# Performance work log

Measured on AMD Instinct MI355X. Metric: run time of the kernel, lower is better.

## Reference

```python
import jax, jax.numpy as jnp
import numpy as np

N = 8192
IN_F = 256
OUT_F = 128


def setup_inputs() -> dict:
    key = jax.random.key(0)
    k1, k2, k3, k4, k5, k6 = jax.random.split(key, 6)
    input = jax.random.normal(k1, (N, IN_F), dtype=jnp.float32)
    adj = jax.random.randint(k2, (N, N), 0, 2, dtype=jnp.int32)
    # xavier-uniform-like init scaled by gain=0.5
    def xavier(k, shape, gain=0.5):
        fan_in, fan_out = shape[0], shape[1]
        lim = gain * np.sqrt(6.0 / (fan_in + fan_out))
        return jax.random.uniform(k, shape, dtype=jnp.float32, minval=-lim, maxval=lim)
    W_s = xavier(k3, (IN_F, OUT_F))
    a_s = xavier(k4, (OUT_F, 1))
    W_n = xavier(k5, (IN_F, OUT_F))
    a_n = xavier(k6, (OUT_F, 1))
    return {"input": input, "adj": adj, "W_s": W_s, "a_s": a_s, "W_n": W_n, "a_n": a_n}


def reference(input, adj, W_s, a_s, W_n, a_n):
    # Projections: [N, out_features]
    h_s = input @ W_s
    h_n = input @ W_n
    # Additive attention logits: e[i, j] = relu((h_s @ a_s)[i] + (h_n @ a_n)[j])
    e = jax.nn.relu((h_s @ a_s) + (h_n @ a_n).T)  # [N, N]
    # Masked softmax over neighbors (dim=1)
    attention = jnp.where(adj > 0, e, jnp.float32(-9e15))
    attention = jax.nn.softmax(attention, axis=1)
    # Self-scaling term (sum of softmax rows, kept for faithfulness)
    attention_sum = jnp.sum(attention, axis=-1, keepdims=True)
    attention_s = 1.0 / (1.0 + attention_sum)
    # Dropout is identity in eval mode (p=0 / training=False)
    h_prime = attention_s * h_s + attention @ h_n
    # concat=True -> elu activation
    return jax.nn.elu(h_prime)
```

## Files before the change

kernel.cpp:

```cpp
#include <hip/hip_runtime.h>
#include <math.h>

#define NN 8192

typedef short short8 __attribute__((ext_vector_type(8)));
typedef float f32x4 __attribute__((ext_vector_type(4)));

__device__ __forceinline__ float eluf(float x) {
  return x > 0.f ? x : (__expf(x) - 1.f);
}
__device__ __forceinline__ unsigned short f2bf(float f) {
  union { float f; unsigned u; } v; v.f = f;
  unsigned r = v.u + 0x7fffu + ((v.u >> 16) & 1u);
  return (unsigned short)(r >> 16);
}
__device__ __forceinline__ unsigned pack4(int4 v, int sh) {
  return ((unsigned)(v.x & 1) << sh) | ((unsigned)(v.y & 1) << (sh + 1)) |
         ((unsigned)(v.z & 1) << (sh + 2)) | ((unsigned)(v.w & 1) << (sh + 3));
}

__global__ __launch_bounds__(256) void k_pre(const float* __restrict__ X,
                                             const int* __restrict__ A,
                                             const float* __restrict__ Ws,
                                             const float* __restrict__ Wn,
                                             const float* __restrict__ as_,
                                             const float* __restrict__ an_,
                                             float* __restrict__ Hs,
                                             unsigned short* __restrict__ HnT,
                                             float* __restrict__ es_out,
                                             float* __restrict__ en_out,
                                             unsigned* __restrict__ P) {
  __shared__ float4 lin4[8 * 64];
  const int bid = blockIdx.x;
  const int q5 = bid / 5, r5 = bid - q5 * 5;
  const int t = threadIdx.x;

  if (r5 == 4) {
    const int row0 = q5 * 32;
#pragma unroll 1
    for (int k = 0; k < 32; ++k) {
      int g = t + k * 256;
      int rr = g >> 8;
      int c8 = g & 255;
      const int4* src = (const int4*)(A + (size_t)(row0 + rr) * NN + c8 * 32);
      int4 v0 = src[0], v1 = src[1], v2 = src[2], v3 = src[3];
      int4 v4 = src[4], v5 = src[5], v6 = src[6], v7 = src[7];
      unsigned w = pack4(v0, 0)  | pack4(v1, 4)  | pack4(v2, 8)  | pack4(v3, 12) |
                   pack4(v4, 16) | pack4(v5, 20) | pack4(v6, 24) | pack4(v7, 28);
      P[(size_t)(row0 + rr) * 256 + c8] = w;
    }
    return;
  }

  const int i0 = (q5 * 4 + r5) * 8;
  const float4* Xg = (const float4*)X + (size_t)i0 * 64;
  lin4[t] = Xg[t];
  lin4[t + 256] = Xg[t + 256];
  __syncthreads();
  const int c = t & 127;
  const int rh = t >> 7;
  float accs[4], accn[4];
#pragma unroll
  for (int r = 0; r < 4; ++r) { accs[r] = 0.f; accn[r] = 0.f; }
  for (int k = 0; k < 256; k += 4) {
    float ws0 = Ws[(k + 0) * 128 + c], ws1 = Ws[(k + 1) * 128 + c];
    float ws2 = Ws[(k + 2) * 128 + c], ws3 = Ws[(k + 3) * 128 + c];
    float wn0 = Wn[(k + 0) * 128 + c], wn1 = Wn[(k + 1) * 128 + c];
    float wn2 = Wn[(k + 2) * 128 + c], wn3 = Wn[(k + 3) * 128 + c];
#pragma unroll
    for (int r = 0; r < 4; ++r) {
      float4 iv = lin4[(rh * 4 + r) * 64 + (k >> 2)];
      accs[r] = fmaf(iv.x, ws0, accs[r]); accs[r] = fmaf(iv.y, ws1, accs[r]);
      accs[r] = fmaf(iv.z, ws2, accs[r]); accs[r] = fmaf(iv.w, ws3, accs[r]);
      accn[r] = fmaf(iv.x, wn0, accn[r]); accn[r] = fmaf(iv.y, wn1, accn[r]);
      accn[r] = fmaf(iv.z, wn2, accn[r]); accn[r] = fmaf(iv.w, wn3, accn[r]);
    }
  }
#pragma unroll
  for (int r = 0; r < 4; ++r)
    Hs[(size_t)(i0 + rh * 4 + r) * 128 + c] = accs[r];
  {
    union { unsigned short us[4]; ushort4 u4; } pk;
#pragma unroll
    for (int r = 0; r < 4; ++r) pk.us[r] = f2bf(accn[r]);
    *(ushort4*)(HnT + (size_t)(i0 >> 3) * 1024 + c * 8 + rh * 4) = pk.u4;
  }
  float* red = (float*)lin4;
  const int wv = t >> 6, ln = t & 63;
  __syncthreads();
  {
    float av = as_[c];
#pragma unroll
    for (int r = 0; r < 4; ++r) red[(rh * 4 + r) * 128 + c] = accs[r] * av;
  }
  __syncthreads();
#pragma unroll
  for (int h = 0; h < 2; ++h) {
    int row = wv * 2 + h;
    float p = red[row * 128 + ln] + red[row * 128 + 64 + ln];
#pragma unroll
    for (int off = 32; off >= 1; off >>= 1) p += __shfl_down(p, off);
    if (ln == 0) es_out[i0 + row] = __expf(p);
  }
  __syncthreads();
  {
    float av = an_[c];
#pragma unroll
    for (int r = 0; r < 4; ++r) red[(rh * 4 + r) * 128 + c] = accn[r] * av;
  }
  __syncthreads();
#pragma unroll
  for (int h = 0; h < 2; ++h) {
    int row = wv * 2 + h;
    float p = red[row * 128 + ln] + red[row * 128 + 64 + ln];
#pragma unroll
    for (int off = 32; off >= 1; off >>= 1) p += __shfl_down(p, off);
    if (ln == 0) en_out[i0 + row] = __expf(p);
  }
}

__global__ __launch_bounds__(512, 4) void k_main(const unsigned* __restrict__ Pk,
                                                 const unsigned short* __restrict__ HnT,
                                                 const float* __restrict__ es_g,
                                                 const float* __restrict__ en_g,
                                                 float* __restrict__ HsOut) {
  __shared__ __align__(16) char smem[49152];
  float* en_lds = (float*)smem;
  unsigned* bits_lds = (unsigned*)(smem + 32768);
  float* cmb = (float*)smem;
  __shared__ float zsh[8][16];
  __shared__ float zf[16];

  const int t = threadIdx.x;
  const int wv = t >> 6;
  const int ln = t & 63;
  const int q = ln >> 4;
  const int m = ln & 15;
  const int row0 = blockIdx.x * 16;

  {
    float4* dst = (float4*)en_lds;
    const float4* s4 = (const float4*)en_g;
#pragma unroll
    for (int k = 0; k < 4; ++k) dst[t + k * 512] = s4[t + k * 512];
#pragma unroll
    for (int k = 0; k < 8; ++k) {
      int g = t + k * 512;
      int rr = g >> 8;
      int c8 = g & 255;
      unsigned w = Pk[(size_t)(row0 + rr) * 256 + c8];
      bits_lds[(c8 >> 5) * 512 + (c8 & 31) * 16 + rr] = w;
    }
  }

  const float sme = es_g[row0 + m];
  const unsigned short* bptr = HnT + ((size_t)(wv * 128 + q) * 128 + m) * 8;
  const float* nvl = en_lds + wv * 1024 + q * 8;
  const unsigned* bts = bits_lds + wv * 512 + m;

  f32x4 acc[8];
#pragma unroll
  for (int ft = 0; ft < 8; ++ft) acc[ft] = (f32x4){0.f, 0.f, 0.f, 0.f};
  float zp = 0.f;

  union Breg { uint4 u; short8 s; };
  Breg breg[8];

  __syncthreads();

  breg[0].u = *(const uint4*)(bptr);       breg[1].u = *(const uint4*)(bptr + 128);
  breg[2].u = *(const uint4*)(bptr + 256); breg[3].u = *(const uint4*)(bptr + 384);
  breg[4].u = *(const uint4*)(bptr + 512); breg[5].u = *(const uint4*)(bptr + 640);
  breg[6].u = *(const uint4*)(bptr + 768); breg[7].u = *(const uint4*)(bptr + 896);

#pragma unroll 2
  for (int tt = 0; tt < 32; ++tt) {
    short8 fr;
    {
      float4 nv0 = *(const float4*)(nvl + tt * 32);
      float4 nv1 = *(const float4*)(nvl + tt * 32 + 4);
      const unsigned bw = bts[tt * 16];
      const unsigned byte = (bw >> (q * 8)) & 0xffu;
      float ev[8] = {nv0.x, nv0.y, nv0.z, nv0.w, nv1.x, nv1.y, nv1.z, nv1.w};
#pragma unroll
      for (int k = 0; k < 8; ++k) {
        float w = ((byte >> k) & 1u) ? fmaxf(sme * ev[k], 1.f) : 0.f;
        zp += w;
        fr[k] = (short)f2bf(w);
      }
    }
    __builtin_amdgcn_s_setprio(1);
    acc[0] = __builtin_amdgcn_mfma_f32_16x16x32_bf16(fr, breg[0].s, acc[0], 0, 0, 0);
    acc[1] = __builtin_amdgcn_mfma_f32_16x16x32_bf16(fr, breg[1].s, acc[1], 0, 0, 0);
    acc[2] = __builtin_amdgcn_mfma_f32_16x16x32_bf16(fr, breg[2].s, acc[2], 0, 0, 0);
    acc[3] = __builtin_amdgcn_mfma_f32_16x16x32_bf16(fr, breg[3].s, acc[3], 0, 0, 0);
    acc[4] = __builtin_amdgcn_mfma_f32_16x16x32_bf16(fr, breg[4].s, acc[4], 0, 0, 0);
    acc[5] = __builtin_amdgcn_mfma_f32_16x16x32_bf16(fr, breg[5].s, acc[5], 0, 0, 0);
    acc[6] = __builtin_amdgcn_mfma_f32_16x16x32_bf16(fr, breg[6].s, acc[6], 0, 0, 0);
    acc[7] = __builtin_amdgcn_mfma_f32_16x16x32_bf16(fr, breg[7].s, acc[7], 0, 0, 0);
    __builtin_amdgcn_s_setprio(0);
    {
      const unsigned short* p = bptr + (size_t)(tt + 1) * 4096;
      breg[0].u = *(const uint4*)(p);       breg[1].u = *(const uint4*)(p + 128);
      breg[2].u = *(const uint4*)(p + 256); breg[3].u = *(const uint4*)(p + 384);
      breg[4].u = *(const uint4*)(p + 512); breg[5].u = *(const uint4*)(p + 640);
      breg[6].u = *(const uint4*)(p + 768); breg[7].u = *(const uint4*)(p + 896);
    }
  }

  {
    float zz = zp;
    zz += __shfl_down(zz, 32);
    zz += __shfl_down(zz, 16);
    if (ln < 16) zsh[wv][ln] = zz;
  }
  __syncthreads();
  if (wv >= 4) {
#pragma unroll
    for (int ft = 0; ft < 8; ++ft)
#pragma unroll
      for (int reg = 0; reg < 4; ++reg)
        cmb[(wv - 4) * 2048 + (q * 4 + reg) * 128 + ft * 16 + m] = acc[ft][reg];
  }
  __syncthreads();
  if (wv < 4) {
#pragma unroll
    for (int ft = 0; ft < 8; ++ft)
#pragma unroll
      for (int reg = 0; reg < 4; ++reg)
        acc[ft][reg] += cmb[wv * 2048 + (q * 4 + reg) * 128 + ft * 16 + m];
  }
  __syncthreads();
  if (wv < 4) {
#pragma unroll
    for (int ft = 0; ft < 8; ++ft)
#pragma unroll
      for (int reg = 0; reg < 4; ++reg)
        cmb[wv * 2048 + (q * 4 + reg) * 128 + ft * 16 + m] = acc[ft][reg];
  }
  if (t < 16) {
    float z = zsh[0][t] + zsh[1][t] + zsh[2][t] + zsh[3][t] +
              zsh[4][t] + zsh[5][t] + zsh[6][t] + zsh[7][t];
    zf[t] = 1.f / z;
  }
  __syncthreads();
  {
    const int row = t >> 5;
    const int f0 = (t & 31) * 4;
    f32x4 ssum = *(const f32x4*)&cmb[row * 128 + f0];
#pragma unroll
    for (int w = 1; w < 4; ++w) ssum += *(const f32x4*)&cmb[w * 2048 + row * 128 + f0];
    const float invz = zf[row];
    const size_t off = (size_t)(row0 + row) * 128 + f0;
    float4 h = *(const float4*)(HsOut + off);
    float4 o;
    o.x = eluf(fmaf(ssum[0], invz, 0.5f * h.x));
    o.y = eluf(fmaf(ssum[1], invz, 0.5f * h.y));
    o.z = eluf(fmaf(ssum[2], invz, 0.5f * h.z));
    o.w = eluf(fmaf(ssum[3], invz, 0.5f * h.w));
    *(float4*)(HsOut + off) = o;
  }
}

extern "C" void kernel_launch(void* const* d_in, const int* in_sizes, int n_in,
                              void* d_out, int out_size, void* d_ws, size_t ws_size,
                              hipStream_t stream) {
  const float* X   = (const float*)d_in[0];
  const int*   A   = (const int*)d_in[1];
  const float* Ws  = (const float*)d_in[2];
  const float* as_ = (const float*)d_in[3];
  const float* Wn  = (const float*)d_in[4];
  const float* an_ = (const float*)d_in[5];
  float* out = (float*)d_out;

  unsigned short* HnT = (unsigned short*)d_ws;
  float* es = (float*)(HnT + (size_t)128 * NN);
  float* en = es + NN;
  unsigned* P = (unsigned*)(en + NN);

  k_pre<<<1280, 256, 0, stream>>>(X, A, Ws, Wn, as_, an_, out, HnT, es, en, P);
  k_main<<<512, 512, 0, stream>>>(P, HnT, es, en, out);
}
```

Baseline: 418.3 us.

## Process 32 rows per block with 1024 threads, reusing B fragments across two row tiles

Each block of k_main now handles 32 output rows with 16 waves arranged as 2 feature halves by 8 column chunks. Each wave reuses its loaded HnT fragments for two 16-row A tiles, which halves global reads of the HnT matrix per output row. The cross-wave reduction becomes a multi-stage tree through LDS with more barriers. The grid shrinks to 256 blocks, which may leave compute units underfilled on a 256-CU part, and the 64KB LDS plus doubled register state may limit occupancy.

Result: no change. 421.5 us (+0.8%).

```diff
diff --git a/kernel.cpp b/kernel.cpp
--- a/kernel.cpp
+++ b/kernel.cpp
@@ -119,137 +119,156 @@
   }
 }
 
-__global__ __launch_bounds__(512, 4) void k_main(const unsigned* __restrict__ Pk,
-                                                 const unsigned short* __restrict__ HnT,
-                                                 const float* __restrict__ es_g,
-                                                 const float* __restrict__ en_g,
-                                                 float* __restrict__ HsOut) {
-  __shared__ __align__(16) char smem[49152];
+__global__ __launch_bounds__(1024, 4) void k_main(const unsigned* __restrict__ Pk,
+                                                  const unsigned short* __restrict__ HnT,
+                                                  const float* __restrict__ es_g,
+                                                  const float* __restrict__ en_g,
+                                                  float* __restrict__ HsOut) {
+  __shared__ __align__(16) char smem[65536];
   float* en_lds = (float*)smem;
   unsigned* bits_lds = (unsigned*)(smem + 32768);
   float* cmb = (float*)smem;
-  __shared__ float zsh[8][16];
-  __shared__ float zf[16];
+  __shared__ float zsh[8][32];
+  __shared__ float zf[32];
 
   const int t = threadIdx.x;
   const int wv = t >> 6;
+  const int fp = wv >> 3;
+  const int jp = wv & 7;
   const int ln = t & 63;
   const int q = ln >> 4;
   const int m = ln & 15;
-  const int row0 = blockIdx.x * 16;
+  const int row0 = blockIdx.x * 32;
 
   {
     float4* dst = (float4*)en_lds;
     const float4* s4 = (const float4*)en_g;
-#pragma unroll
-    for (int k = 0; k < 4; ++k) dst[t + k * 512] = s4[t + k * 512];
+    dst[t] = s4[t];
+    dst[t + 1024] = s4[t + 1024];
 #pragma unroll
     for (int k = 0; k < 8; ++k) {
-      int g = t + k * 512;
+      int g = t + k * 1024;
       int rr = g >> 8;
       int c8 = g & 255;
       unsigned w = Pk[(size_t)(row0 + rr) * 256 + c8];
-      bits_lds[(c8 >> 5) * 512 + (c8 & 31) * 16 + rr] = w;
-    }
-  }
-
-  const float sme = es_g[row0 + m];
-  const unsigned short* bptr = HnT + ((size_t)(wv * 128 + q) * 128 + m) * 8;
-  const float* nvl = en_lds + wv * 1024 + q * 8;
-  const unsigned* bts = bits_lds + wv * 512 + m;
-
-  f32x4 acc[8];
-#pragma unroll
-  for (int ft = 0; ft < 8; ++ft) acc[ft] = (f32x4){0.f, 0.f, 0.f, 0.f};
-  float zp = 0.f;
+      bits_lds[(c8 >> 5) * 1024 + (c8 & 31) * 32 + rr] = w;
+    }
+  }
+
+  const float sme0 = es_g[row0 + m];
+  const float sme1 = es_g[row0 + 16 + m];
+  const unsigned short* bptr = HnT + ((size_t)(jp * 128 + q) * 128 + fp * 64 + m) * 8;
+  const float* nvl = en_lds + jp * 1024 + q * 8;
+  const unsigned* bts = bits_lds + jp * 1024 + m;
+
+  f32x4 acc0[4], acc1[4];
+#pragma unroll
+  for (int ftl = 0; ftl < 4; ++ftl) {
+    acc0[ftl] = (f32x4){0.f, 0.f, 0.f, 0.f};
+    acc1[ftl] = (f32x4){0.f, 0.f, 0.f, 0.f};
+  }
+  float zp0 = 0.f, zp1 = 0.f;
 
   union Breg { uint4 u; short8 s; };
-  Breg breg[8];
-
-  __syncthreads();
-
-  breg[0].u = *(const uint4*)(bptr);       breg[1].u = *(const uint4*)(bptr + 128);
-  breg[2].u = *(const uint4*)(bptr + 256); breg[3].u = *(const uint4*)(bptr + 384);
-  breg[4].u = *(const uint4*)(bptr + 512); breg[5].u = *(const uint4*)(bptr + 640);
-  breg[6].u = *(const uint4*)(bptr + 768); breg[7].u = *(const uint4*)(bptr + 896);
+  Breg breg[4];
+
+  __syncthreads();
+
+  breg[0].u = *(const uint4*)(bptr);
+  breg[1].u = *(const uint4*)(bptr + 128);
+  breg[2].u = *(const uint4*)(bptr + 256);
+  breg[3].u = *(const uint4*)(bptr + 384);
 
 #pragma unroll 2
   for (int tt = 0; tt < 32; ++tt) {
-    short8 fr;
+    short8 fr0, fr1;
     {
       float4 nv0 = *(const float4*)(nvl + tt * 32);
       float4 nv1 = *(const float4*)(nvl + tt * 32 + 4);
-      const unsigned bw = bts[tt * 16];
-      const unsigned byte = (bw >> (q * 8)) & 0xffu;
+      const unsigned bw0 = bts[tt * 32];
+      const unsigned bw1 = bts[tt * 32 + 16];
+      const unsigned byte0 = (bw0 >> (q * 8)) & 0xffu;
+      const unsigned byte1 = (bw1 >> (q * 8)) & 0xffu;
       float ev[8] = {nv0.x, nv0.y, nv0.z, nv0.w, nv1.x, nv1.y, nv1.z, nv1.w};
 #pragma unroll
       for (int k = 0; k < 8; ++k) {
-        float w = ((byte >> k) & 1u) ? fmaxf(sme * ev[k], 1.f) : 0.f;
-        zp += w;
-        fr[k] = (short)f2bf(w);
+        float w0 = ((byte0 >> k) & 1u) ? fmaxf(sme0 * ev[k], 1.f) : 0.f;
+        float w1 = ((byte1 >> k) & 1u) ? fmaxf(sme1 * ev[k], 1.f) : 0.f;
+        zp0 += w0; zp1 += w1;
+        fr0[k] = (short)f2bf(w0);
+        fr1[k] = (short)f2bf(w1);
       }
     }
     __builtin_amdgcn_s_setprio(1);
-    acc[0] = __builtin_amdgcn_mfma_f32_16x16x32_bf16(fr, breg[0].s, acc[0], 0, 0, 0);
-    acc[1] = __builtin_amdgcn_mfma_f32_16x16x32_bf16(fr, breg[1].s, acc[1], 0, 0, 0);
-    acc[2] = __builtin_amdgcn_mfma_f32_16x16x32_bf16(fr, breg[2].s, acc[2], 0, 0, 0);
-    acc[3] = __builtin_amdgcn_mfma_f32_16x16x32_bf16(fr, breg[3].s, acc[3], 0, 0, 0);
-    acc[4] = __builtin_amdgcn_mfma_f32_16x16x32_bf16(fr, breg[4].s, acc[4], 0, 0, 0);
-    acc[5] = __builtin_amdgcn_mfma_f32_16x16x32_bf16(fr, breg[5].s, acc[5], 0, 0, 0);
-    acc[6] = __builtin_amdgcn_mfma_f32_16x16x32_bf16(fr, breg[6].s, acc[6], 0, 0, 0);
-    acc[7] = __builtin_amdgcn_mfma_f32_16x16x32_bf16(fr, breg[7].s, acc[7], 0, 0, 0);
+    acc0[0] = __builtin_amdgcn_mfma_f32_16x16x32_bf16(fr0, breg[0].s, acc0[0], 0, 0, 0);
+    acc1[0] = __builtin_amdgcn_mfma_f32_16x16x32_bf16(fr1, breg[0].s, acc1[0], 0, 0, 0);
+    acc0[1] = __builtin_amdgcn_mfma_f32_16x16x32_bf16(fr0, breg[1].s, acc0[1], 0, 0, 0);
+    acc1[1] = __builtin_amdgcn_mfma_f32_16x16x32_bf16(fr1, breg[1].s, acc1[1], 0, 0, 0);
+    acc0[2] = __builtin_amdgcn_mfma_f32_16x16x32_bf16(fr0, breg[2].s, acc0[2], 0, 0, 0);
+    acc1[2] = __builtin_amdgcn_mfma_f32_16x16x32_bf16(fr1, breg[2].s, acc1[2], 0, 0, 0);
+    acc0[3] = __builtin_amdgcn_mfma_f32_16x16x32_bf16(fr0, breg[3].s, acc0[3], 0, 0, 0);
+    acc1[3] = __builtin_amdgcn_mfma_f32_16x16x32_bf16(fr1, breg[3].s, acc1[3], 0, 0, 0);
     __builtin_amdgcn_s_setprio(0);
     {
       const unsigned short* p = bptr + (size_t)(tt + 1) * 4096;
-      breg[0].u = *(const uint4*)(p);       breg[1].u = *(const uint4*)(p + 128);
-      breg[2].u = *(const uint4*)(p + 256); breg[3].u = *(const uint4*)(p + 384);
-      breg[4].u = *(const uint4*)(p + 512); breg[5].u = *(const uint4*)(p + 640);
-      breg[6].u = *(const uint4*)(p + 768); breg[7].u = *(const uint4*)(p + 896);
-    }
-  }
-
-  {
-    float zz = zp;
-    zz += __shfl_down(zz, 32);
-    zz += __shfl_down(zz, 16);
-    if (ln < 16) zsh[wv][ln] = zz;
-  }
-  __syncthreads();
-  if (wv >= 4) {
-#pragma unroll
-    for (int ft = 0; ft < 8; ++ft)
-#pragma unroll
-      for (int reg = 0; reg < 4; ++reg)
-        cmb[(wv - 4) * 2048 + (q * 4 + reg) * 128 + ft * 16 + m] = acc[ft][reg];
-  }
-  __syncthreads();
-  if (wv < 4) {
-#pragma unroll
-    for (int ft = 0; ft < 8; ++ft)
-#pragma unroll
-      for (int reg = 0; reg < 4; ++reg)
-        acc[ft][reg] += cmb[wv * 2048 + (q * 4 + reg) * 128 + ft * 16 + m];
-  }
-  __syncthreads();
-  if (wv < 4) {
-#pragma unroll
-    for (int ft = 0; ft < 8; ++ft)
-#pragma unroll
-      for (int reg = 0; reg < 4; ++reg)
-        cmb[wv * 2048 + (q * 4 + reg) * 128 + ft * 16 + m] = acc[ft][reg];
-  }
-  if (t < 16) {
+      breg[0].u = *(const uint4*)(p);
+      breg[1].u = *(const uint4*)(p + 128);
+      breg[2].u = *(const uint4*)(p + 256);
+      breg[3].u = *(const uint4*)(p + 384);
+    }
+  }
+
+  {
+    float zz0 = zp0, zz1 = zp1;
+    zz0 += __shfl_down(zz0, 32); zz0 += __shfl_down(zz0, 16);
+    zz1 += __shfl_down(zz1, 32); zz1 += __shfl_down(zz1, 16);
+    if (fp == 0 && ln < 16) { zsh[jp][m] = zz0; zsh[jp][16 + m] = zz1; }
+  }
+  __syncthreads();
+
+#define DUMP_SLOT(S)                                                        \
+  {                                                                         \
+    float* d = cmb + (S) * 2048 + q * 256 + m;                              \
+    _Pragma("unroll") for (int ftl = 0; ftl < 4; ++ftl)                     \
+      _Pragma("unroll") for (int reg = 0; reg < 4; ++reg) {                 \
+        d[reg * 64 + ftl * 16] = acc0[ftl][reg];                            \
+        d[1024 + reg * 64 + ftl * 16] = acc1[ftl][reg];                     \
+      }                                                                     \
+  }
+#define ADD_SLOT(S)                                                         \
+  {                                                                         \
+    const float* d = cmb + (S) * 2048 + q * 256 + m;                        \
+    _Pragma("unroll") for (int ftl = 0; ftl < 4; ++ftl)                     \
+      _Pragma("unroll") for (int reg = 0; reg < 4; ++reg) {                 \
+        acc0[ftl][reg] += d[reg * 64 + ftl * 16];                           \
+        acc1[ftl][reg] += d[1024 + reg * 64 + ftl * 16];                    \
+      }                                                                     \
+  }
+  if (jp >= 4) DUMP_SLOT(fp * 4 + (jp - 4));
+  __syncthreads();
+  if (jp < 4) ADD_SLOT(fp * 4 + jp);
+  if (t < 32) {
     float z = zsh[0][t] + zsh[1][t] + zsh[2][t] + zsh[3][t] +
               zsh[4][t] + zsh[5][t] + zsh[6][t] + zsh[7][t];
     zf[t] = 1.f / z;
   }
   __syncthreads();
+  if (jp == 2 || jp == 3) DUMP_SLOT(fp * 2 + (jp - 2));
+  __syncthreads();
+  if (jp < 2) ADD_SLOT(fp * 2 + jp);
+  __syncthreads();
+  if (jp == 1) DUMP_SLOT(fp);
+  __syncthreads();
+  if (jp == 0) { ADD_SLOT(fp); DUMP_SLOT(fp); }
+  __syncthreads();
+#undef DUMP_SLOT
+#undef ADD_SLOT
+
   {
     const int row = t >> 5;
     const int f0 = (t & 31) * 4;
-    f32x4 ssum = *(const f32x4*)&cmb[row * 128 + f0];
-#pragma unroll
-    for (int w = 1; w < 4; ++w) ssum += *(const f32x4*)&cmb[w * 2048 + row * 128 + f0];
+    const int fpx = f0 >> 6;
+    f32x4 ssum = *(const f32x4*)&cmb[fpx * 2048 + row * 64 + (f0 & 63)];
     const float invz = zf[row];
     const size_t off = (size_t)(row0 + row) * 128 + f0;
     float4 h = *(const float4*)(HsOut + off);
@@ -279,5 +298,5 @@
   unsigned* P = (unsigned*)(en + NN);
 
   k_pre<<<1280, 256, 0, stream>>>(X, A, Ws, Wn, as_, an_, out, HnT, es, en, P);
-  k_main<<<512, 512, 0, stream>>>(P, HnT, es, en, out);
-}
+  k_main<<<256, 1024, 0, stream>>>(P, HnT, es, en, out);
+}
```
